# Performance work log

Measured on AMD Instinct MI355X. Metric: run time of the kernel, lower is better.

## Reference

```python
import jax, jax.numpy as jnp
import numpy as np

B, D, F, P = 65536, 256, 512, 256


def setup_inputs() -> dict:
    key = jax.random.key(0)
    k_x, k_f, k_p, k_a, k_b, k_t = jax.random.split(key, 6)
    x = jax.random.normal(k_x, (B, D), dtype=jnp.float32)
    # reset_parameters: uniform(-0.27, 1)
    features = jax.random.uniform(k_f, (F, D), dtype=jnp.float32, minval=-0.27, maxval=1.0)
    prototypes = jax.random.uniform(k_p, (P, D), dtype=jnp.float32, minval=-0.27, maxval=1.0)
    # alpha/beta/theta init to zeros in the module; use small random values so the
    # output is non-trivial for kernel correctness checking.
    alpha = jax.random.normal(k_a, (1,), dtype=jnp.float32) * 0.1
    beta = jax.random.normal(k_b, (1,), dtype=jnp.float32) * 0.1
    theta = jax.random.normal(k_t, (1,), dtype=jnp.float32) * 0.1
    return {"x": x, "features": features, "prototypes": prototypes,
            "alpha": alpha, "beta": beta, "theta": theta}


def reference(x, features, prototypes, alpha, beta, theta):
    # Shared projections
    x_features = x @ features.T                 # [B, F]
    p_features = prototypes @ features.T        # [P, F]
    x_present = jax.nn.relu(x_features)         # [B, F]
    p_present = jax.nn.relu(p_features)         # [P, F]
    x_weighted = x_features * x_present         # [B, F]
    p_weighted = p_features * p_present         # [P, F]

    # Tversky terms
    common = x_weighted @ p_weighted.T                          # [B, P]
    x_weighted_sum = jnp.sum(x_weighted, axis=1, keepdims=True)  # [B, 1]
    x_p_interaction = x_weighted @ p_present.T                  # [B, P]
    x_distinctive = x_weighted_sum - x_p_interaction            # [B, P]
    p_weighted_sum = jnp.sum(p_weighted, axis=1)[None, :]        # [1, P]
    x_p_weighted_interaction = x_present @ p_weighted.T         # [B, P]
    p_distinctive = p_weighted_sum - x_p_weighted_interaction   # [B, P]

    return theta * common - alpha * x_distinctive - beta * p_distinctive
```

## Files before the change

### kernel.cpp

```cpp
#include <hip/hip_runtime.h>
#include <cstdint>
#include <cstddef>

#define Bsz 65536
#define Dsz 256
#define Fsz 512
#define Psz 256

typedef __attribute__((ext_vector_type(8))) short short8;
typedef __attribute__((ext_vector_type(4))) short short4v;
typedef __attribute__((ext_vector_type(4))) float float4v;
typedef __attribute__((ext_vector_type(16))) float float16v;
typedef __attribute__((ext_vector_type(4))) unsigned uint4v;

__device__ inline short f2bf(float f) {
    unsigned u = __builtin_bit_cast(unsigned, f);
    u = (u + 0x7FFFu + ((u >> 16) & 1u)) >> 16;
    return (short)u;
}
__device__ inline float bf2f(short s) {
    unsigned u = ((unsigned)(unsigned short)s) << 16;
    return __builtin_bit_cast(float, u);
}
__device__ inline unsigned cvt_pk_bf16(float lo, float hi) {
    unsigned r;
    asm("v_cvt_pk_bf16_f32 %0, %1, %2" : "=v"(r) : "v"(lo), "v"(hi));
    return r;
}
__device__ inline void gl_lds16(const short* g, short* lds) {
    __builtin_amdgcn_global_load_lds((const __attribute__((address_space(1))) unsigned*)g,
                                     (__attribute__((address_space(3))) unsigned*)lds,
                                     16, 0, 0);
}


#define SBPITCH 136

__global__ __launch_bounds__(256, 2) void k_pre(
    const float* __restrict__ prototypes, const float* __restrict__ features,
    const float* __restrict__ alpha_p, const float* __restrict__ beta_p,
    const float* __restrict__ theta_p,
    short* __restrict__ featbB, short* __restrict__ pab, float* __restrict__ pws_part)
{
    __shared__ char lds[65536 + 17408];
    short* FB = (short*)lds;
    short* As = (short*)(lds + 65536);
    short* Sb = (short*)(lds + 65536);

    const int t = threadIdx.x;
    const int w = t >> 6, lane = t & 63, l15 = lane & 15, l4 = lane >> 4;
    const int rowg = blockIdx.x >> 2, nc = blockIdx.x & 3;
    const float alpha = *alpha_p, beta = *beta_p, theta = *theta_p;

    #pragma unroll
    for (int it = 0; it < 16; ++it) {
        int u = it * 256 + t;
        int ftl = u >> 10, dtl = (u >> 6) & 15, ln = u & 63;
        const float* src = features + (size_t)(nc * 128 + ftl * 32 + (ln & 31)) * Dsz
                         + dtl * 16 + (ln >> 5) * 8;
        float4v v0 = *(const float4v*)src;
        float4v v1 = *(const float4v*)(src + 4);
        uint4v uv;
        uv.x = cvt_pk_bf16(v0.x, v0.y);
        uv.y = cvt_pk_bf16(v0.z, v0.w);
        uv.z = cvt_pk_bf16(v1.x, v1.y);
        uv.w = cvt_pk_bf16(v1.z, v1.w);
        short8 sv = __builtin_bit_cast(short8, uv);
        *(short8*)&FB[u * 8] = sv;
        if (rowg == 0) {
            int go = (((nc * 4 + ftl) * 16 + dtl) * 64 + ln) * 8;
            *(short8*)&featbB[go] = sv;
        }
    }

    float4v acc[2][4];
    #pragma unroll
    for (int a = 0; a < 2; ++a)
        #pragma unroll
        for (int b = 0; b < 4; ++b) acc[a][b] = (float4v){0.f, 0.f, 0.f, 0.f};

    const float* pbase = prototypes + (size_t)rowg * 64 * Dsz;

    for (int kc = 0; kc < 4; ++kc) {
        __syncthreads();
        #pragma unroll
        for (int j = 0; j < 4; ++j) {
            int idx = j * 1024 + t * 4;
            int r = idx >> 6, c = idx & 63;
            float4v v = *(const float4v*)(pbase + (size_t)r * Dsz + kc * 64 + c);
            int unit = r * 8 + ((c >> 3) ^ (r & 7));
            short4v s4; s4.x = f2bf(v.x); s4.y = f2bf(v.y); s4.z = f2bf(v.z); s4.w = f2bf(v.w);
            *(short4v*)((char*)As + unit * 16 + (c & 7) * 2) = s4;
        }
        __syncthreads();
        #pragma unroll
        for (int kk = 0; kk < 2; ++kk) {
            short8 af[2], bfr[4];
            const int k8 = kk * 4 + l4;
            #pragma unroll
            for (int tm = 0; tm < 2; ++tm) {
                int m = (w & 1) * 32 + tm * 16 + l15;
                af[tm] = *(const short8*)&As[(m * 8 + (k8 ^ (m & 7))) * 8];
            }
            #pragma unroll
            for (int tn = 0; tn < 4; ++tn) {
                int fl = ((w >> 1) * 4 + tn) * 16 + l15;
                int dtl = kc * 4 + kk * 2 + (l4 >> 1);
                int lnp = (fl & 31) + 32 * (l4 & 1);
                bfr[tn] = *(const short8*)&FB[(((fl >> 5) * 16 + dtl) * 64 + lnp) * 8];
            }
            #pragma unroll
            for (int tm = 0; tm < 2; ++tm)
                #pragma unroll
                for (int tn = 0; tn < 4; ++tn)
                    acc[tm][tn] = __builtin_amdgcn_mfma_f32_16x16x32_bf16(af[tm], bfr[tn], acc[tm][tn], 0, 0, 0);
        }
    }
    __syncthreads();
    #pragma unroll
    for (int tm = 0; tm < 2; ++tm)
        #pragma unroll
        for (int tn = 0; tn < 4; ++tn)
            #pragma unroll
            for (int r = 0; r < 4; ++r) {
                int row = (w & 1) * 32 + tm * 16 + l4 * 4 + r;
                int col = (w >> 1) * 64 + tn * 16 + l15;
                Sb[row * SBPITCH + col] = f2bf(acc[tm][tn][r]);
            }
    __syncthreads();
    #pragma unroll
    for (int rep = 0; rep < 4; ++rep) {
        int u = rep * 256 + t;
        int row = u >> 4, i = u & 15;
        short8 sv = *(const short8*)&Sb[row * SBPITCH + i * 8];
        uint4v u0, u1;
        float sum = 0.f;
        #pragma unroll
        for (int e = 0; e < 8; ++e) {
            float pf = bf2f(sv[e]);
            float pp = fmaxf(pf, 0.f);
            float pw = pf * pp;
            float a0 = theta * pw + alpha * (pp - 1.f);
            float b0 = beta * pw;
            sum += pw;
            unsigned pk = cvt_pk_bf16(a0, b0);
            if (e < 4) u0[e] = pk; else u1[e - 4] = pk;
        }
        int p = rowg * 64 + row;
        int c = 4 * nc + (i >> 2), s2 = i & 3, pt = p >> 5;
        int base = ((c * 4 + s2) * 8 + pt) * 512;
        *(short8*)&pab[base + (p & 31) * 8] = __builtin_bit_cast(short8, u0);
        *(short8*)&pab[base + ((p & 31) + 32) * 8] = __builtin_bit_cast(short8, u1);
        #pragma unroll
        for (int mk = 1; mk < 16; mk <<= 1) sum += __shfl_xor(sum, mk, 64);
        if (l15 == 0) pws_part[nc * 256 + p] = -beta * sum;
    }
}

__global__ __launch_bounds__(256, 2) void k_main(
    const float* __restrict__ x, const short* __restrict__ featbB,
    const short* __restrict__ pab, const float* __restrict__ pws_part,
    float* __restrict__ out)
{
    __shared__ short FBL[2][8192];
    __shared__ float EXC[4096];

    const int t = threadIdx.x;
    const int w = t >> 6, lane = t & 63, l31 = lane & 31, h = lane >> 5;
    const int mt = w & 1, pth = w >> 1;
    const size_t row0 = (size_t)blockIdx.x * 64;
    const int lane8 = lane * 8;
    const int excW = (mt * 2 + pth) * 1024 + lane * 4;
    const int excR = (mt * 2 + (pth ^ 1)) * 1024 + lane * 4;

    auto stage_fb = [&](int cn, int buf) {
        const short* src = featbB + cn * 8192 + lane8;
        #pragma unroll
        for (int i = 0; i < 4; ++i)
            gl_lds16(src + (4 * w + i) * 512, &FBL[buf][(4 * w + i) * 512]);
    };

    stage_fb(0, 0);
    __builtin_amdgcn_sched_barrier(0);

    short8 xf[8];
    {
        const float* xr = x + (row0 + mt * 32 + l31) * Dsz + pth * 128 + h * 8;
        #pragma unroll
        for (int i = 0; i < 8; ++i) {
            float4v v0 = *(const float4v*)(xr + i * 16);
            float4v v1 = *(const float4v*)(xr + i * 16 + 4);
            uint4v uv;
            uv.x = cvt_pk_bf16(v0.x, v0.y);
            uv.y = cvt_pk_bf16(v0.z, v0.w);
            uv.z = cvt_pk_bf16(v1.x, v1.y);
            uv.w = cvt_pk_bf16(v1.z, v1.w);
            xf[i] = __builtin_bit_cast(short8, uv);
        }
    }

    float16v acc[4];
    #pragma unroll
    for (int a = 0; a < 4; ++a)
        #pragma unroll
        for (int e = 0; e < 16; ++e) acc[a][e] = 0.f;

    __syncthreads();

    #pragma unroll 1
    for (int c = 0; c < 16; ++c) {
        const int cur = c & 1;

        if (c) __syncthreads();

        const short* pb = pab + (size_t)c * 16384 + lane8;
        short8 PA[16];
        #pragma unroll
        for (int k = 0; k < 16; ++k)
            PA[k] = *(const short8*)(pb + ((k >> 2) * 8 + pth * 4 + (k & 3)) * 512);
        if (c < 15) stage_fb(c + 1, cur ^ 1);
        __builtin_amdgcn_sched_barrier(0);

        float16v Ca, Cb;
        #pragma unroll
        for (int e = 0; e < 16; ++e) { Ca[e] = 0.f; Cb[e] = 0.f; }
        #pragma unroll
        for (int g = 0; g < 2; ++g) {
            short8 fbf[4];
            #pragma unroll
            for (int i = 0; i < 4; ++i)
                fbf[i] = *(const short8*)&FBL[cur][(pth * 8 + g * 4 + i) * 512 + lane8];
            __builtin_amdgcn_s_setprio(1);
            #pragma unroll
            for (int i = 0; i < 4; ++i) {
                if (i & 1) Cb = __builtin_amdgcn_mfma_f32_32x32x16_bf16(fbf[i], xf[g * 4 + i], Cb, 0, 0, 0);
                else       Ca = __builtin_amdgcn_mfma_f32_32x32x16_bf16(fbf[i], xf[g * 4 + i], Ca, 0, 0, 0);
            }
            __builtin_amdgcn_s_setprio(0);
        }
        float16v Cp;
        #pragma unroll
        for (int e = 0; e < 16; ++e) Cp[e] = Ca[e] + Cb[e];

        #pragma unroll
        for (int q = 0; q < 4; ++q)
            *(float4v*)&EXC[excW + q * 256] =
                (float4v){Cp[4 * q], Cp[4 * q + 1], Cp[4 * q + 2], Cp[4 * q + 3]};

        __builtin_amdgcn_sched_barrier(0);
        asm volatile("s_waitcnt lgkmcnt(0)" ::: "memory");
        __builtin_amdgcn_s_barrier();
        __builtin_amdgcn_sched_barrier(0);

        float16v C1;
        #pragma unroll
        for (int q = 0; q < 4; ++q) {
            float4v o = *(const float4v*)&EXC[excR + q * 256];
            C1[4 * q]     = Cp[4 * q]     + o.x;
            C1[4 * q + 1] = Cp[4 * q + 1] + o.y;
            C1[4 * q + 2] = Cp[4 * q + 2] + o.z;
            C1[4 * q + 3] = Cp[4 * q + 3] + o.w;
        }

        #pragma unroll
        for (int s = 0; s < 4; ++s) {
            uint4v uf;
            #pragma unroll
            for (int q = 0; q < 4; ++q) {
                float xv = C1[4 * s + q];
                float xp = fmaxf(xv, 0.f);
                uf[q] = cvt_pk_bf16(xv * xp, xp);
            }
            short8 A2f = __builtin_bit_cast(short8, uf);
            __builtin_amdgcn_s_setprio(1);
            #pragma unroll
            for (int ptl = 0; ptl < 4; ++ptl)
                acc[ptl] = __builtin_amdgcn_mfma_f32_32x32x16_bf16(A2f, PA[s * 4 + ptl], acc[ptl], 0, 0, 0);
            __builtin_amdgcn_s_setprio(0);
        }
    }

    #pragma unroll
    for (int ptl = 0; ptl < 4; ++ptl) {
        int pcol = (pth * 4 + ptl) * 32 + l31;
        float pn = pws_part[pcol] + pws_part[256 + pcol] + pws_part[512 + pcol] + pws_part[768 + pcol];
        #pragma unroll
        for (int r = 0; r < 16; ++r) {
            size_t m = row0 + mt * 32 + (r & 3) + 8 * (r >> 2) + 4 * h;
            out[m * Psz + pcol] = acc[ptl][r] + pn;
        }
    }
}

extern "C" void kernel_launch(void* const* d_in, const int* in_sizes, int n_in,
                              void* d_out, int out_size, void* d_ws, size_t ws_size,
                              hipStream_t stream) {
    const float* x          = (const float*)d_in[0];
    const float* features   = (const float*)d_in[1];
    const float* prototypes = (const float*)d_in[2];
    const float* alpha      = (const float*)d_in[3];
    const float* beta       = (const float*)d_in[4];
    const float* theta      = (const float*)d_in[5];
    float* out = (float*)d_out;

    char* ws = (char*)d_ws;
    short* featbB   = (short*)(ws);
    short* pab      = (short*)(ws + 262144);
    float* pws_part = (float*)(ws + 786432);

    hipLaunchKernelGGL(k_pre,  dim3(16),   dim3(256), 0, stream,
                       prototypes, features, alpha, beta, theta, featbB, pab, pws_part);
    hipLaunchKernelGGL(k_main, dim3(1024), dim3(256), 0, stream,
                       x, featbB, pab, pws_part, out);
}
```

Before: 181.2 us.

## Prefetch next chunk's prototype and feature tiles after the second-stage MFMAs

The global loads of the next chunk's prototype operands (PA) and the LDS staging of the next feature buffer now start at the end of each iteration, after the second-stage MFMAs. A vmcnt-bounded wait plus barrier replaces the `__syncthreads` at the top of the loop, so those loads overlap the next chunk's first-stage MFMAs. The two interleaved partial accumulators are merged into one serial MFMA chain. The bf16 packing for all four slices now runs before a single batched block of MFMAs. The aim is to hide global load latency and cut synchronization cost, at the price of a longer dependent MFMA chain in the first stage.

```diff
diff --git a/kernel.cpp b/kernel.cpp
--- a/kernel.cpp
+++ b/kernel.cpp
@@ -180,9 +180,6 @@
             gl_lds16(src + (4 * w + i) * 512, &FBL[buf][(4 * w + i) * 512]);
     };
 
-    stage_fb(0, 0);
-    __builtin_amdgcn_sched_barrier(0);
-
     short8 xf[8];
     {
         const float* xr = x + (row0 + mt * 32 + l31) * Dsz + pth * 128 + h * 8;
@@ -205,25 +202,27 @@
         #pragma unroll
         for (int e = 0; e < 16; ++e) acc[a][e] = 0.f;
 
-    __syncthreads();
+    short8 PA[16];
+    __builtin_amdgcn_sched_barrier(0);
+    stage_fb(0, 0);
+    {
+        const short* pb0 = pab + lane8;
+        #pragma unroll
+        for (int k = 0; k < 16; ++k)
+            PA[k] = *(const short8*)(pb0 + ((k >> 2) * 8 + pth * 4 + (k & 3)) * 512);
+    }
+    __builtin_amdgcn_sched_barrier(0);
+    asm volatile("s_waitcnt vmcnt(16)" ::: "memory");
+    __builtin_amdgcn_s_barrier();
+    __builtin_amdgcn_sched_barrier(0);
 
     #pragma unroll 1
     for (int c = 0; c < 16; ++c) {
         const int cur = c & 1;
 
-        if (c) __syncthreads();
-
-        const short* pb = pab + (size_t)c * 16384 + lane8;
-        short8 PA[16];
-        #pragma unroll
-        for (int k = 0; k < 16; ++k)
-            PA[k] = *(const short8*)(pb + ((k >> 2) * 8 + pth * 4 + (k & 3)) * 512);
-        if (c < 15) stage_fb(c + 1, cur ^ 1);
-        __builtin_amdgcn_sched_barrier(0);
-
-        float16v Ca, Cb;
-        #pragma unroll
-        for (int e = 0; e < 16; ++e) { Ca[e] = 0.f; Cb[e] = 0.f; }
+        float16v Cp;
+        #pragma unroll
+        for (int e = 0; e < 16; ++e) Cp[e] = 0.f;
         #pragma unroll
         for (int g = 0; g < 2; ++g) {
             short8 fbf[4];
@@ -232,15 +231,10 @@
                 fbf[i] = *(const short8*)&FBL[cur][(pth * 8 + g * 4 + i) * 512 + lane8];
             __builtin_amdgcn_s_setprio(1);
             #pragma unroll
-            for (int i = 0; i < 4; ++i) {
-                if (i & 1) Cb = __builtin_amdgcn_mfma_f32_32x32x16_bf16(fbf[i], xf[g * 4 + i], Cb, 0, 0, 0);
-                else       Ca = __builtin_amdgcn_mfma_f32_32x32x16_bf16(fbf[i], xf[g * 4 + i], Ca, 0, 0, 0);
-            }
+            for (int i = 0; i < 4; ++i)
+                Cp = __builtin_amdgcn_mfma_f32_32x32x16_bf16(fbf[i], xf[g * 4 + i], Cp, 0, 0, 0);
             __builtin_amdgcn_s_setprio(0);
         }
-        float16v Cp;
-        #pragma unroll
-        for (int e = 0; e < 16; ++e) Cp[e] = Ca[e] + Cb[e];
 
         #pragma unroll
         for (int q = 0; q < 4; ++q)
@@ -252,31 +246,38 @@
         __builtin_amdgcn_s_barrier();
         __builtin_amdgcn_sched_barrier(0);
 
-        float16v C1;
-        #pragma unroll
-        for (int q = 0; q < 4; ++q) {
-            float4v o = *(const float4v*)&EXC[excR + q * 256];
-            C1[4 * q]     = Cp[4 * q]     + o.x;
-            C1[4 * q + 1] = Cp[4 * q + 1] + o.y;
-            C1[4 * q + 2] = Cp[4 * q + 2] + o.z;
-            C1[4 * q + 3] = Cp[4 * q + 3] + o.w;
-        }
-
+        short8 A2[4];
         #pragma unroll
         for (int s = 0; s < 4; ++s) {
+            float4v o = *(const float4v*)&EXC[excR + s * 256];
             uint4v uf;
             #pragma unroll
             for (int q = 0; q < 4; ++q) {
-                float xv = C1[4 * s + q];
+                float xv = Cp[4 * s + q] + ((const float*)&o)[q];
                 float xp = fmaxf(xv, 0.f);
                 uf[q] = cvt_pk_bf16(xv * xp, xp);
             }
-            short8 A2f = __builtin_bit_cast(short8, uf);
-            __builtin_amdgcn_s_setprio(1);
+            A2[s] = __builtin_bit_cast(short8, uf);
+        }
+
+        __builtin_amdgcn_s_setprio(1);
+        #pragma unroll
+        for (int s = 0; s < 4; ++s)
             #pragma unroll
             for (int ptl = 0; ptl < 4; ++ptl)
-                acc[ptl] = __builtin_amdgcn_mfma_f32_32x32x16_bf16(A2f, PA[s * 4 + ptl], acc[ptl], 0, 0, 0);
-            __builtin_amdgcn_s_setprio(0);
+                acc[ptl] = __builtin_amdgcn_mfma_f32_32x32x16_bf16(A2[s], PA[s * 4 + ptl], acc[ptl], 0, 0, 0);
+        __builtin_amdgcn_s_setprio(0);
+
+        if (c < 15) {
+            stage_fb(c + 1, cur ^ 1);
+            const short* pbn = pab + (size_t)(c + 1) * 16384 + lane8;
+            #pragma unroll
+            for (int k = 0; k < 16; ++k)
+                PA[k] = *(const short8*)(pbn + ((k >> 2) * 8 + pth * 4 + (k & 3)) * 512);
+            __builtin_amdgcn_sched_barrier(0);
+            asm volatile("s_waitcnt vmcnt(16)" ::: "memory");
+            __builtin_amdgcn_s_barrier();
+            __builtin_amdgcn_sched_barrier(0);
         }
     }
 
```

Measured after the change: 185.1 us. 2.2% more time.
